# Kernel optimization log

Hardware: AMD Instinct MI355X
Metric: run time of the kernel (lower is better)

Reference implementation:

```python
import jax, jax.numpy as jnp
import numpy as np

D_IN = 512
D_OUT = 512
NUM_HEADS = 8
HEAD_DIM = D_OUT // NUM_HEADS


def setup_inputs() -> dict:
    key = jax.random.key(0)
    ks = jax.random.split(key, 6)
    b, t, n = 4, 32, 256
    scale = 1.0 / np.sqrt(D_IN)
    return {
        "x": jax.random.normal(ks[0], (b, t, n, D_IN), dtype=jnp.float32),
        "Wq": jax.random.normal(ks[1], (D_IN, D_OUT), dtype=jnp.float32) * scale,
        "Wk": jax.random.normal(ks[2], (D_IN, D_OUT), dtype=jnp.float32) * scale,
        "Wv": jax.random.normal(ks[3], (D_IN, D_OUT), dtype=jnp.float32) * scale,
        "Wo": jax.random.normal(ks[4], (D_OUT, D_OUT), dtype=jnp.float32) * scale,
        "bo": jax.random.normal(ks[5], (D_OUT,), dtype=jnp.float32) * 0.01,
    }


def reference(x, Wq, Wk, Wv, Wo, bo):
    b, t, n, _ = x.shape
    h, hd = NUM_HEADS, HEAD_DIM
    # QKV projections (no bias, qkv_bias=False)
    q = (x @ Wq).reshape(b, t, n, h, hd)
    k = (x @ Wk).reshape(b, t, n, h, hd)
    v = (x @ Wv).reshape(b, t, n, h, hd)
    # attention over tokens, per (batch, timestamp, head)
    scores = jnp.einsum('btqhd,btkhd->bthqk', q, k) / np.sqrt(hd).astype(jnp.float32)
    weights = jax.nn.softmax(scores, axis=-1)
    # dropout p=0.0 (eval / deterministic reference) -> identity
    ctx = jnp.einsum('bthqk,btkhd->btqhd', weights, v).reshape(b, t, n, D_OUT)
    return ctx @ Wo + bo
```

## Files before the change

kernel.cpp:

```cpp
#include <hip/hip_runtime.h>
#include <hip/hip_bf16.h>

typedef __attribute__((ext_vector_type(8))) short bf16x8;
typedef __attribute__((ext_vector_type(4))) float f32x4;

#define MFMA_16x16x32(a,b,c) __builtin_amdgcn_mfma_f32_16x16x32_bf16((a),(b),(c),0,0,0)

__device__ __forceinline__ unsigned short f2bf(float f){
  unsigned int u = __float_as_uint(f);
  u += 0x7FFFu + ((u >> 16) & 1u);
  return (unsigned short)(u >> 16);
}

__device__ __forceinline__ unsigned int cvtpk_bf16(float lo, float hi){
  unsigned int r;
  asm("v_cvt_pk_bf16_f32 %0, %1, %2" : "=v"(r) : "v"(lo), "v"(hi));
  return r;
}

__device__ __forceinline__ void async16(const void* g, void* l){
  __builtin_amdgcn_global_load_lds((const __attribute__((address_space(1))) void*)g,
                                   (__attribute__((address_space(3))) void*)l,
                                   16, 0, 0);
}

#define FENCE asm volatile("" ::: "memory")
#define BARR  do{ FENCE; __builtin_amdgcn_s_barrier(); FENCE; }while(0)

__global__ __launch_bounds__(256) void convert_x_kernel(const float* __restrict__ x,
                                                        unsigned short* __restrict__ xb, int n4){
  int idx = blockIdx.x*256 + threadIdx.x;
  int stride = gridDim.x*256;
  for (int i = idx; i < n4; i += stride){
    float4 v = reinterpret_cast<const float4*>(x)[i];
    ushort4 o;
    o.x = f2bf(v.x); o.y = f2bf(v.y); o.z = f2bf(v.z); o.w = f2bf(v.w);
    reinterpret_cast<ushort4*>(xb)[i] = o;
  }
}

__global__ __launch_bounds__(256) void prep_weights(const float* __restrict__ Wq,
                                                    const float* __restrict__ Wk,
                                                    const float* __restrict__ Wv,
                                                    const float* __restrict__ Wo,
                                                    unsigned short* __restrict__ WqkvT,
                                                    unsigned short* __restrict__ WoT){
  int idx = blockIdx.x*256 + threadIdx.x;
  int stride = gridDim.x*256;
  const int T1 = 1536*512;
  const int total = T1 + 512*512;
  for (int o = idx; o < total; o += stride){
    if (o < T1){
      int n = o >> 9, k = o & 511;
      const float* W = (n < 512) ? Wq : ((n < 1024) ? Wk : Wv);
      WqkvT[o] = f2bf(W[k*512 + (n & 511)]);
    } else {
      int o2 = o - T1;
      int n = o2 >> 9, k = o2 & 511;
      WoT[o2] = f2bf(Wo[k*512 + n]);
    }
  }
}

template<bool BIAS, bool OUTBF16>
__global__ __launch_bounds__(512, 2) void gemm8(const unsigned short* __restrict__ A,
                                                const unsigned short* __restrict__ Bt,
                                                float* __restrict__ Cf, unsigned short* __restrict__ Cb,
                                                const float* __restrict__ bias,
                                                int K, int NB, int ldc){
  __shared__ __attribute__((aligned(16))) char ldsA[2][32768];
  __shared__ __attribute__((aligned(16))) char ldsB[2][32768];
  const int tid = threadIdx.x;
  const int lane = tid & 63, w = tid >> 6;
  const int wr = w >> 2, wc = w & 3;
  const int l15 = lane & 15, lhi = lane >> 4;
  const int xorv = (l15 & 7) << 4;

  const int cpx = gridDim.x >> 3;
  const int bid = (blockIdx.x & 7) * cpx + (blockIdx.x >> 3);
  const int bm = bid / NB, bn = bid % NB;

  const int row0 = tid >> 3;
  const int srcb = ((tid & 7) << 4) ^ ((row0 & 7) << 4);
  const size_t rK2 = (size_t)K * 2;
  const char* Ab = (const char*)(A + (size_t)(bm*256 + row0) * K) + srcb;
  const char* Bb = (const char*)(Bt + (size_t)(bn*256 + row0) * K) + srcb;

#define STG_A(p,h,kt) do{ \
    async16(Ab + (size_t)((h)*128)*rK2      + (size_t)(kt)*2, ldsA[p] + (h)*16384 +        w*1024); \
    async16(Ab + (size_t)((h)*128 + 64)*rK2 + (size_t)(kt)*2, ldsA[p] + (h)*16384 + 8192 + w*1024); }while(0)
#define STG_B(p,h,kt) do{ \
    async16(Bb + (size_t)((h)*128)*rK2      + (size_t)(kt)*2, ldsB[p] + (h)*16384 +        w*1024); \
    async16(Bb + (size_t)((h)*128 + 64)*rK2 + (size_t)(kt)*2, ldsB[p] + (h)*16384 + 8192 + w*1024); }while(0)

#define LDAF(p, mh) do{ _Pragma("unroll") for (int f=0;f<4;++f){ \
    const char* base_ = ldsA[p] + (wr*128 + ((mh)*4+f)*16 + l15)*128; \
    af[f][0] = *reinterpret_cast<const bf16x8*>(base_ + (((lhi<<4))      ^ xorv)); \
    af[f][1] = *reinterpret_cast<const bf16x8*>(base_ + ((64 + (lhi<<4)) ^ xorv)); } }while(0)
#define LDBF(dst, p, nh) do{ _Pragma("unroll") for (int n2=0;n2<2;++n2){ \
    const char* base_ = ldsB[p] + (wc*64 + ((nh)*2+n2)*16 + l15)*128; \
    dst[n2][0] = *reinterpret_cast<const bf16x8*>(base_ + (((lhi<<4))      ^ xorv)); \
    dst[n2][1] = *reinterpret_cast<const bf16x8*>(base_ + ((64 + (lhi<<4)) ^ xorv)); } }while(0)
#define MFQ(mh, nh, B_) do{ _Pragma("unroll") for (int f=0;f<4;++f) \
    _Pragma("unroll") for (int n2=0;n2<2;++n2) \
    _Pragma("unroll") for (int kk=0;kk<2;++kk) \
      acc[(mh)*4+f][(nh)*2+n2] = MFMA_16x16x32(af[f][kk], B_[n2][kk], acc[(mh)*4+f][(nh)*2+n2]); }while(0)

  f32x4 acc[8][4];
  const f32x4 fzero = {0.f,0.f,0.f,0.f};
  #pragma unroll
  for (int i=0;i<8;++i)
    #pragma unroll
    for (int j=0;j<4;++j) acc[i][j] = fzero;
  bf16x8 af[4][2], bf0[2][2], bfc[2][2];
  const int nt = K >> 6;

  STG_B(0,0,0);  STG_B(0,1,0);  STG_A(0,0,0);  STG_A(0,1,0);
  STG_B(1,0,64); STG_B(1,1,64);
  asm volatile("s_waitcnt vmcnt(4)" ::: "memory");
  __builtin_amdgcn_s_barrier(); FENCE;

  for (int t = 0; t < nt; ++t){
    const int p = t & 1, o = p ^ 1;
    const int kt1 = (t+1) << 6, kt2 = (t+2) << 6;
    LDAF(p, 0); LDBF(bf0, p, 0);
    if (t+1 < nt) STG_A(o, 0, kt1);
    BARR;
    __builtin_amdgcn_s_setprio(1); MFQ(0, 0, bf0); __builtin_amdgcn_s_setprio(0);
    BARR;
    LDBF(bfc, p, 1);
    if (t+1 < nt) STG_A(o, 1, kt1);
    BARR;
    __builtin_amdgcn_s_setprio(1); MFQ(0, 1, bfc); __builtin_amdgcn_s_setprio(0);
    BARR;
    LDAF(p, 1);
    if (t+2 < nt) STG_B(p, 0, kt2);
    BARR;
    __builtin_amdgcn_s_setprio(1); MFQ(1, 1, bfc); __builtin_amdgcn_s_setprio(0);
    BARR;
    if (t+2 < nt) STG_B(p, 1, kt2);
    BARR;
    __builtin_amdgcn_s_setprio(1); MFQ(1, 0, bf0); __builtin_amdgcn_s_setprio(0);
    if (t+1 < nt){
      if (t+2 < nt) asm volatile("s_waitcnt vmcnt(4)" ::: "memory");
      else          asm volatile("s_waitcnt vmcnt(0)" ::: "memory");
      __builtin_amdgcn_s_barrier(); FENCE;
    }
  }

  #pragma unroll
  for (int mi=0;mi<8;++mi){
    const int r = bm*256 + wr*128 + mi*16 + lhi*4;
    #pragma unroll
    for (int ni=0;ni<4;++ni){
      const int cc = bn*256 + wc*64 + ni*16 + l15;
      float bv = 0.f;
      if (BIAS) bv = bias[cc];
      #pragma unroll
      for (int i=0;i<4;++i){
        float v = acc[mi][ni][i] + bv;
        if (OUTBF16) Cb[(size_t)(r+i)*ldc + cc] = f2bf(v);
        else         Cf[(size_t)(r+i)*ldc + cc] = v;
      }
    }
  }
#undef STG_A
#undef STG_B
#undef LDAF
#undef LDBF
#undef MFQ
}

__global__ __launch_bounds__(256) void attn_kernel(const unsigned short* __restrict__ qkv,
                                                   unsigned short* __restrict__ ctx){
  __shared__ __attribute__((aligned(16))) unsigned short Ks[256*64];
  __shared__ __attribute__((aligned(16))) unsigned short Vst[64*264];

  const int bid = blockIdx.x;
  const int h = bid & 7, bt = bid >> 3;
  const int r0 = bt << 8;
  const int tid = threadIdx.x;
  const int lane = tid & 63, w = tid >> 6;
  const int l15 = lane & 15, lhi = lane >> 4;
  const char* qkvB = (const char*)qkv;
  const f32x4 fzero = {0.f,0.f,0.f,0.f};

  bf16x8 qf[4][2];
  #pragma unroll
  for (int st=0; st<4; ++st){
    int q0 = w*64 + st*16;
    #pragma unroll
    for (int kk=0; kk<2; ++kk)
      qf[st][kk] = *reinterpret_cast<const bf16x8*>(
          qkvB + ((size_t)(r0 + q0 + l15)*1536 + h*64 + kk*32 + lhi*8)*2);
  }

  #pragma unroll
  for (int j=0;j<8;++j){
    int c = (w*8+j)*64 + lane;
    int tok = c >> 3;
    int src = ((c & 7) << 4) ^ ((tok & 7) << 4);
    async16(qkvB + ((size_t)(r0 + tok)*1536 + 512 + h*64)*2 + src,
            (char*)Ks + ((w*8+j) << 10));
  }
  {
    const char* vbase = qkvB + ((size_t)(r0 + tid)*1536 + 1024 + h*64)*2;
    #pragma unroll
    for (int j=0;j<8;++j){
      bf16x8 vv = *reinterpret_cast<const bf16x8*>(vbase + (j<<4));
      #pragma unroll
      for (int e=0;e<8;++e)
        Vst[(j*8+e)*264 + tid] = (unsigned short)vv[e];
    }
  }
  __syncthreads();

  const int ga2 = (lhi & 1) << 1;
  const int lA = l15 + (ga2 << 4);
  const int lB = lA + 16;
  const bool odd = (lhi >> 1) != 0;

  #pragma unroll
  for (int st=0; st<4; ++st){
    const int q0 = w*64 + st*16;

    f32x4 S[16];
    #pragma unroll
    for (int t=0;t<16;++t) S[t] = fzero;
    #pragma unroll
    for (int kk=0;kk<2;++kk){
      #pragma unroll
      for (int t=0;t<16;++t){
        int tok = t*16 + l15;
        int off = tok*128 + (((kk<<6) + (lhi<<4)) ^ ((tok & 7) << 4));
        bf16x8 kf = *reinterpret_cast<const bf16x8*>((const char*)Ks + off);
        S[t] = MFMA_16x16x32(kf, qf[st][kk], S[t]);
      }
    }

    float m = S[0][0];
    #pragma unroll
    for (int t=0;t<16;++t)
      #pragma unroll
      for (int i=0;i<4;++i) m = fmaxf(m, S[t][i]);
    m = fmaxf(m, __shfl_xor(m, 16));
    m = fmaxf(m, __shfl_xor(m, 32));

    float l = 0.f;
    unsigned int P2[32];
    #pragma unroll
    for (int t=0;t<16;++t){
      float p0 = __expf((S[t][0] - m) * 0.125f);
      float p1 = __expf((S[t][1] - m) * 0.125f);
      float p2 = __expf((S[t][2] - m) * 0.125f);
      float p3 = __expf((S[t][3] - m) * 0.125f);
      l += (p0 + p1) + (p2 + p3);
      P2[2*t]   = cvtpk_bf16(p0, p1);
      P2[2*t+1] = cvtpk_bf16(p2, p3);
    }
    l += __shfl_xor(l, 16);
    l += __shfl_xor(l, 32);
    float rl = 1.0f / l;

    f32x4 O[4];
    #pragma unroll
    for (int dt=0;dt<4;++dt) O[dt] = fzero;
    #pragma unroll
    for (int s=0;s<8;++s){
      unsigned int a0e = __shfl((int)P2[4*s+0], lA), a0o = __shfl((int)P2[4*s+2], lA);
      unsigned int a1e = __shfl((int)P2[4*s+1], lA), a1o = __shfl((int)P2[4*s+3], lA);
      unsigned int b0e = __shfl((int)P2[4*s+0], lB), b0o = __shfl((int)P2[4*s+2], lB);
      unsigned int b1e = __shfl((int)P2[4*s+1], lB), b1o = __shfl((int)P2[4*s+3], lB);
      unsigned int u0 = odd ? a0o : a0e;
      unsigned int u1 = odd ? a1o : a1e;
      unsigned int u2 = odd ? b0o : b0e;
      unsigned int u3 = odd ? b1o : b1e;
      bf16x8 pa;
      reinterpret_cast<unsigned int*>(&pa)[0] = u0;
      reinterpret_cast<unsigned int*>(&pa)[1] = u1;
      reinterpret_cast<unsigned int*>(&pa)[2] = u2;
      reinterpret_cast<unsigned int*>(&pa)[3] = u3;
      #pragma unroll
      for (int dt=0;dt<4;++dt){
        bf16x8 vb = *reinterpret_cast<const bf16x8*>(&Vst[(dt*16 + l15)*264 + s*32 + 8*lhi]);
        O[dt] = MFMA_16x16x32(pa, vb, O[dt]);
      }
    }

    float rl4[4];
    #pragma unroll
    for (int i=0;i<4;++i) rl4[i] = __shfl(rl, lhi*4 + i);
    #pragma unroll
    for (int dt=0;dt<4;++dt){
      int col = h*64 + dt*16 + l15;
      #pragma unroll
      for (int i=0;i<4;++i){
        int row = r0 + q0 + lhi*4 + i;
        ctx[(size_t)row*512 + col] = f2bf(O[dt][i] * rl4[i]);
      }
    }
  }
}

extern "C" void kernel_launch(void* const* d_in, const int* in_sizes, int n_in,
                              void* d_out, int out_size, void* d_ws, size_t ws_size,
                              hipStream_t stream) {
  const float* x  = (const float*)d_in[0];
  const float* Wq = (const float*)d_in[1];
  const float* Wk = (const float*)d_in[2];
  const float* Wv = (const float*)d_in[3];
  const float* Wo = (const float*)d_in[4];
  const float* bo = (const float*)d_in[5];
  float* out = (float*)d_out;

  char* ws = (char*)d_ws;
  unsigned short* xb    = (unsigned short*)ws;
  unsigned short* qkv   = (unsigned short*)(ws + 33554432);
  unsigned short* WqkvT = (unsigned short*)(ws + 134217728);
  unsigned short* WoT   = (unsigned short*)(ws + 135790592);
  unsigned short* ctx   = xb;

  convert_x_kernel<<<2048, 256, 0, stream>>>(x, xb, 16777216/4);
  prep_weights<<<1024, 256, 0, stream>>>(Wq, Wk, Wv, Wo, WqkvT, WoT);
  gemm8<false, true><<<768, 512, 0, stream>>>(xb, WqkvT, nullptr, qkv, nullptr, 512, 6, 1536);
  attn_kernel<<<1024, 256, 0, stream>>>(qkv, ctx);
  gemm8<true, false><<<256, 512, 0, stream>>>(ctx, WoT, out, nullptr, bo, 512, 2, 512);
}
```

Baseline: 168.4 us.

## Merge conversion kernels and use smaller-tile GEMM for output projection

Merges the x conversion and the weight transpose/convert into one kernel, saving a launch. Replaces the output-projection gemm8 (256 blocks of 512 threads) with a new 128x128-tile gemm_bt launched as 1024 blocks of 256 threads. The smaller tiles are meant to spread the output GEMM across more CUs. The new GEMM is single-buffered, with a sync between load and compute, so it gives up the pipelining the original kernel likely had.

```diff
diff --git a/kernel.cpp b/kernel.cpp
--- a/kernel.cpp
+++ b/kernel.cpp
@@ -27,26 +27,23 @@
 #define FENCE asm volatile("" ::: "memory")
 #define BARR  do{ FENCE; __builtin_amdgcn_s_barrier(); FENCE; }while(0)
 
-__global__ __launch_bounds__(256) void convert_x_kernel(const float* __restrict__ x,
-                                                        unsigned short* __restrict__ xb, int n4){
+__global__ __launch_bounds__(256) void convert_all(const float* __restrict__ x,
+                                                   const float* __restrict__ Wq,
+                                                   const float* __restrict__ Wk,
+                                                   const float* __restrict__ Wv,
+                                                   const float* __restrict__ Wo,
+                                                   unsigned short* __restrict__ xb,
+                                                   unsigned short* __restrict__ WqkvT,
+                                                   unsigned short* __restrict__ WoT){
   int idx = blockIdx.x*256 + threadIdx.x;
   int stride = gridDim.x*256;
+  const int n4 = 16777216/4;
   for (int i = idx; i < n4; i += stride){
     float4 v = reinterpret_cast<const float4*>(x)[i];
     ushort4 o;
     o.x = f2bf(v.x); o.y = f2bf(v.y); o.z = f2bf(v.z); o.w = f2bf(v.w);
     reinterpret_cast<ushort4*>(xb)[i] = o;
   }
-}
-
-__global__ __launch_bounds__(256) void prep_weights(const float* __restrict__ Wq,
-                                                    const float* __restrict__ Wk,
-                                                    const float* __restrict__ Wv,
-                                                    const float* __restrict__ Wo,
-                                                    unsigned short* __restrict__ WqkvT,
-                                                    unsigned short* __restrict__ WoT){
-  int idx = blockIdx.x*256 + threadIdx.x;
-  int stride = gridDim.x*256;
   const int T1 = 1536*512;
   const int total = T1 + 512*512;
   for (int o = idx; o < total; o += stride){
@@ -169,6 +166,89 @@
 #undef LDAF
 #undef LDBF
 #undef MFQ
+}
+
+template<bool BIAS, bool OUTBF16>
+__global__ __launch_bounds__(256) void gemm_bt(const unsigned short* __restrict__ A,
+                                               const unsigned short* __restrict__ Bt,
+                                               float* __restrict__ Cf, unsigned short* __restrict__ Cb,
+                                               const float* __restrict__ bias,
+                                               int M, int N, int K, int ldc){
+  __shared__ __attribute__((aligned(16))) unsigned short As[128*64];
+  __shared__ __attribute__((aligned(16))) unsigned short Bs[128*64];
+  const int tid = threadIdx.x;
+  const int lane = tid & 63;
+  const int w = tid >> 6;
+  const int l15 = lane & 15, lhi = lane >> 4;
+  const int NB = N >> 7;
+  const int bm = blockIdx.x / NB;
+  const int bn = blockIdx.x % NB;
+  const int wr = w >> 1, wc = w & 1;
+  const f32x4 fzero = {0.f,0.f,0.f,0.f};
+
+  f32x4 acc[4][4];
+  #pragma unroll
+  for (int a=0;a<4;++a)
+    #pragma unroll
+    for (int b=0;b<4;++b) acc[a][b] = fzero;
+
+  for (int kt = 0; kt < K; kt += 64){
+    #pragma unroll
+    for (int j=0;j<4;++j){
+      int c = (w*4+j)*64 + lane;
+      int row = c >> 3;
+      int src = ((c & 7) << 4) ^ ((row & 7) << 4);
+      async16((const char*)(A + (size_t)(bm*128 + row)*K + kt) + src,
+              (char*)As + ((w*4+j) << 10));
+    }
+    #pragma unroll
+    for (int j=0;j<4;++j){
+      int c = (w*4+j)*64 + lane;
+      int row = c >> 3;
+      int src = ((c & 7) << 4) ^ ((row & 7) << 4);
+      async16((const char*)(Bt + (size_t)(bn*128 + row)*K + kt) + src,
+              (char*)Bs + ((w*4+j) << 10));
+    }
+    __syncthreads();
+    #pragma unroll
+    for (int kk=0;kk<2;++kk){
+      bf16x8 af[4], bfr[4];
+      #pragma unroll
+      for (int mi=0;mi<4;++mi){
+        int m = wr*64 + mi*16 + l15;
+        int off = m*128 + (((kk<<6) + (lhi<<4)) ^ ((m & 7) << 4));
+        af[mi] = *reinterpret_cast<const bf16x8*>((const char*)As + off);
+      }
+      #pragma unroll
+      for (int ni=0;ni<4;++ni){
+        int n = wc*64 + ni*16 + l15;
+        int off = n*128 + (((kk<<6) + (lhi<<4)) ^ ((n & 7) << 4));
+        bfr[ni] = *reinterpret_cast<const bf16x8*>((const char*)Bs + off);
+      }
+      #pragma unroll
+      for (int mi=0;mi<4;++mi)
+        #pragma unroll
+        for (int ni=0;ni<4;++ni)
+          acc[mi][ni] = MFMA_16x16x32(af[mi], bfr[ni], acc[mi][ni]);
+    }
+    __syncthreads();
+  }
+  #pragma unroll
+  for (int mi=0;mi<4;++mi){
+    int r = bm*128 + wr*64 + mi*16 + lhi*4;
+    #pragma unroll
+    for (int ni=0;ni<4;++ni){
+      int cc = bn*128 + wc*64 + ni*16 + l15;
+      float bv = 0.f;
+      if (BIAS) bv = bias[cc];
+      #pragma unroll
+      for (int i=0;i<4;++i){
+        float v = acc[mi][ni][i] + bv;
+        if (OUTBF16) Cb[(size_t)(r+i)*ldc + cc] = f2bf(v);
+        else         Cf[(size_t)(r+i)*ldc + cc] = v;
+      }
+    }
+  }
 }
 
 __global__ __launch_bounds__(256) void attn_kernel(const unsigned short* __restrict__ qkv,
@@ -320,9 +400,9 @@
   unsigned short* WoT   = (unsigned short*)(ws + 135790592);
   unsigned short* ctx   = xb;
 
-  convert_x_kernel<<<2048, 256, 0, stream>>>(x, xb, 16777216/4);
-  prep_weights<<<1024, 256, 0, stream>>>(Wq, Wk, Wv, Wo, WqkvT, WoT);
+  convert_all<<<2048, 256, 0, stream>>>(x, Wq, Wk, Wv, Wo, xb, WqkvT, WoT);
   gemm8<false, true><<<768, 512, 0, stream>>>(xb, WqkvT, nullptr, qkv, nullptr, 512, 6, 1536);
   attn_kernel<<<1024, 256, 0, stream>>>(qkv, ctx);
-  gemm8<true, false><<<256, 512, 0, stream>>>(ctx, WoT, out, nullptr, bo, 512, 2, 512);
-}
+  gemm_bt<true, false><<<1024, 256, 0, stream>>>(ctx, WoT, out, nullptr, bo,
+                                                 32768, 512, 512, 512);
+}
```

New measurement: 172.6 us. 1.02x slower.

## Shrink GEMM tiles to 128x128 with 4 waves and fuse conversion kernels

Applied to the files above, without the earlier changes.

Replaces the 256x256-tile, 8-wave GEMM with a 128x128-tile, 4-wave version that has a simpler two-phase pipeline per K step and fewer barriers. Grids grow to 3072 and 1024 blocks to improve load balance and occupancy across CUs. It also merges the x conversion and weight preparation into one launch. The trade-off is less data reuse per tile and more global/L2 traffic.

```diff
diff --git a/kernel.cpp b/kernel.cpp
--- a/kernel.cpp
+++ b/kernel.cpp
@@ -26,27 +26,26 @@
 
 #define FENCE asm volatile("" ::: "memory")
 #define BARR  do{ FENCE; __builtin_amdgcn_s_barrier(); FENCE; }while(0)
-
-__global__ __launch_bounds__(256) void convert_x_kernel(const float* __restrict__ x,
-                                                        unsigned short* __restrict__ xb, int n4){
+#define BARRL do{ asm volatile("s_waitcnt lgkmcnt(0)" ::: "memory"); \
+                  __builtin_amdgcn_s_barrier(); FENCE; }while(0)
+
+__global__ __launch_bounds__(256) void convert_all(const float* __restrict__ x,
+                                                   const float* __restrict__ Wq,
+                                                   const float* __restrict__ Wk,
+                                                   const float* __restrict__ Wv,
+                                                   const float* __restrict__ Wo,
+                                                   unsigned short* __restrict__ xb,
+                                                   unsigned short* __restrict__ WqkvT,
+                                                   unsigned short* __restrict__ WoT){
   int idx = blockIdx.x*256 + threadIdx.x;
   int stride = gridDim.x*256;
+  const int n4 = 16777216/4;
   for (int i = idx; i < n4; i += stride){
     float4 v = reinterpret_cast<const float4*>(x)[i];
     ushort4 o;
     o.x = f2bf(v.x); o.y = f2bf(v.y); o.z = f2bf(v.z); o.w = f2bf(v.w);
     reinterpret_cast<ushort4*>(xb)[i] = o;
   }
-}
-
-__global__ __launch_bounds__(256) void prep_weights(const float* __restrict__ Wq,
-                                                    const float* __restrict__ Wk,
-                                                    const float* __restrict__ Wv,
-                                                    const float* __restrict__ Wo,
-                                                    unsigned short* __restrict__ WqkvT,
-                                                    unsigned short* __restrict__ WoT){
-  int idx = blockIdx.x*256 + threadIdx.x;
-  int stride = gridDim.x*256;
   const int T1 = 1536*512;
   const int total = T1 + 512*512;
   for (int o = idx; o < total; o += stride){
@@ -63,16 +62,16 @@
 }
 
 template<bool BIAS, bool OUTBF16>
-__global__ __launch_bounds__(512, 2) void gemm8(const unsigned short* __restrict__ A,
+__global__ __launch_bounds__(256, 2) void gemm4(const unsigned short* __restrict__ A,
                                                 const unsigned short* __restrict__ Bt,
                                                 float* __restrict__ Cf, unsigned short* __restrict__ Cb,
                                                 const float* __restrict__ bias,
                                                 int K, int NB, int ldc){
-  __shared__ __attribute__((aligned(16))) char ldsA[2][32768];
-  __shared__ __attribute__((aligned(16))) char ldsB[2][32768];
+  __shared__ __attribute__((aligned(16))) char ldsA[2][16384];
+  __shared__ __attribute__((aligned(16))) char ldsB[2][16384];
   const int tid = threadIdx.x;
   const int lane = tid & 63, w = tid >> 6;
-  const int wr = w >> 2, wc = w & 3;
+  const int wr = w >> 1, wc = w & 1;
   const int l15 = lane & 15, lhi = lane >> 4;
   const int xorv = (l15 & 7) << 4;
 
@@ -83,77 +82,65 @@
   const int row0 = tid >> 3;
   const int srcb = ((tid & 7) << 4) ^ ((row0 & 7) << 4);
   const size_t rK2 = (size_t)K * 2;
-  const char* Ab = (const char*)(A + (size_t)(bm*256 + row0) * K) + srcb;
-  const char* Bb = (const char*)(Bt + (size_t)(bn*256 + row0) * K) + srcb;
-
-#define STG_A(p,h,kt) do{ \
-    async16(Ab + (size_t)((h)*128)*rK2      + (size_t)(kt)*2, ldsA[p] + (h)*16384 +        w*1024); \
-    async16(Ab + (size_t)((h)*128 + 64)*rK2 + (size_t)(kt)*2, ldsA[p] + (h)*16384 + 8192 + w*1024); }while(0)
-#define STG_B(p,h,kt) do{ \
-    async16(Bb + (size_t)((h)*128)*rK2      + (size_t)(kt)*2, ldsB[p] + (h)*16384 +        w*1024); \
-    async16(Bb + (size_t)((h)*128 + 64)*rK2 + (size_t)(kt)*2, ldsB[p] + (h)*16384 + 8192 + w*1024); }while(0)
-
-#define LDAF(p, mh) do{ _Pragma("unroll") for (int f=0;f<4;++f){ \
-    const char* base_ = ldsA[p] + (wr*128 + ((mh)*4+f)*16 + l15)*128; \
-    af[f][0] = *reinterpret_cast<const bf16x8*>(base_ + (((lhi<<4))      ^ xorv)); \
-    af[f][1] = *reinterpret_cast<const bf16x8*>(base_ + ((64 + (lhi<<4)) ^ xorv)); } }while(0)
+  const char* Ab = (const char*)(A + (size_t)(bm*128 + row0) * K) + srcb;
+  const char* Bb = (const char*)(Bt + (size_t)(bn*128 + row0) * K) + srcb;
+
+#define STG_A(p,kt) do{ _Pragma("unroll") for (int j=0;j<4;++j) \
+    async16(Ab + (size_t)(j*32)*rK2 + (size_t)(kt)*2, ldsA[p] + j*4096 + w*1024); }while(0)
+#define STG_B(p,kt) do{ _Pragma("unroll") for (int j=0;j<4;++j) \
+    async16(Bb + (size_t)(j*32)*rK2 + (size_t)(kt)*2, ldsB[p] + j*4096 + w*1024); }while(0)
+
+#define LDAF(p) do{ _Pragma("unroll") for (int f=0;f<4;++f){ \
+    const char* base_ = ldsA[p] + (wr*64 + f*16 + l15)*128; \
+    const int m_ = wr*64 + f*16 + l15; \
+    af[f][0] = *reinterpret_cast<const bf16x8*>(base_ + (((lhi<<4))      ^ ((m_&7)<<4))); \
+    af[f][1] = *reinterpret_cast<const bf16x8*>(base_ + ((64 + (lhi<<4)) ^ ((m_&7)<<4))); } }while(0)
 #define LDBF(dst, p, nh) do{ _Pragma("unroll") for (int n2=0;n2<2;++n2){ \
-    const char* base_ = ldsB[p] + (wc*64 + ((nh)*2+n2)*16 + l15)*128; \
-    dst[n2][0] = *reinterpret_cast<const bf16x8*>(base_ + (((lhi<<4))      ^ xorv)); \
-    dst[n2][1] = *reinterpret_cast<const bf16x8*>(base_ + ((64 + (lhi<<4)) ^ xorv)); } }while(0)
-#define MFQ(mh, nh, B_) do{ _Pragma("unroll") for (int f=0;f<4;++f) \
+    const int n_ = wc*64 + ((nh)*2+n2)*16 + l15; \
+    const char* base_ = ldsB[p] + n_*128; \
+    dst[n2][0] = *reinterpret_cast<const bf16x8*>(base_ + (((lhi<<4))      ^ ((n_&7)<<4))); \
+    dst[n2][1] = *reinterpret_cast<const bf16x8*>(base_ + ((64 + (lhi<<4)) ^ ((n_&7)<<4))); } }while(0)
+#define MFQ(nh, B_) do{ _Pragma("unroll") for (int f=0;f<4;++f) \
     _Pragma("unroll") for (int n2=0;n2<2;++n2) \
     _Pragma("unroll") for (int kk=0;kk<2;++kk) \
-      acc[(mh)*4+f][(nh)*2+n2] = MFMA_16x16x32(af[f][kk], B_[n2][kk], acc[(mh)*4+f][(nh)*2+n2]); }while(0)
-
-  f32x4 acc[8][4];
+      acc[f][(nh)*2+n2] = MFMA_16x16x32(af[f][kk], B_[n2][kk], acc[f][(nh)*2+n2]); }while(0)
+
+  f32x4 acc[4][4];
   const f32x4 fzero = {0.f,0.f,0.f,0.f};
   #pragma unroll
-  for (int i=0;i<8;++i)
+  for (int i=0;i<4;++i)
     #pragma unroll
     for (int j=0;j<4;++j) acc[i][j] = fzero;
   bf16x8 af[4][2], bf0[2][2], bfc[2][2];
   const int nt = K >> 6;
 
-  STG_B(0,0,0);  STG_B(0,1,0);  STG_A(0,0,0);  STG_A(0,1,0);
-  STG_B(1,0,64); STG_B(1,1,64);
+  STG_A(0,0); STG_B(0,0); STG_B(1,64);
   asm volatile("s_waitcnt vmcnt(4)" ::: "memory");
   __builtin_amdgcn_s_barrier(); FENCE;
 
   for (int t = 0; t < nt; ++t){
     const int p = t & 1, o = p ^ 1;
     const int kt1 = (t+1) << 6, kt2 = (t+2) << 6;
-    LDAF(p, 0); LDBF(bf0, p, 0);
-    if (t+1 < nt) STG_A(o, 0, kt1);
+    LDAF(p); LDBF(bf0, p, 0); LDBF(bfc, p, 1);
+    if (t+1 < nt) STG_A(o, kt1);
     BARR;
-    __builtin_amdgcn_s_setprio(1); MFQ(0, 0, bf0); __builtin_amdgcn_s_setprio(0);
-    BARR;
-    LDBF(bfc, p, 1);
-    if (t+1 < nt) STG_A(o, 1, kt1);
-    BARR;
-    __builtin_amdgcn_s_setprio(1); MFQ(0, 1, bfc); __builtin_amdgcn_s_setprio(0);
-    BARR;
-    LDAF(p, 1);
-    if (t+2 < nt) STG_B(p, 0, kt2);
-    BARR;
-    __builtin_amdgcn_s_setprio(1); MFQ(1, 1, bfc); __builtin_amdgcn_s_setprio(0);
-    BARR;
-    if (t+2 < nt) STG_B(p, 1, kt2);
-    BARR;
-    __builtin_amdgcn_s_setprio(1); MFQ(1, 0, bf0); __builtin_amdgcn_s_setprio(0);
+    __builtin_amdgcn_s_setprio(1); MFQ(0, bf0); __builtin_amdgcn_s_setprio(0);
+    BARRL;
+    if (t+2 < nt) STG_B(p, kt2);
+    __builtin_amdgcn_s_setprio(1); MFQ(1, bfc); __builtin_amdgcn_s_setprio(0);
     if (t+1 < nt){
-      if (t+2 < nt) asm volatile("s_waitcnt vmcnt(4)" ::: "memory");
-      else          asm volatile("s_waitcnt vmcnt(0)" ::: "memory");
+      if (t+2 < nt) asm volatile("s_waitcnt vmcnt(4) lgkmcnt(0)" ::: "memory");
+      else          asm volatile("s_waitcnt vmcnt(0) lgkmcnt(0)" ::: "memory");
       __builtin_amdgcn_s_barrier(); FENCE;
     }
   }
 
   #pragma unroll
-  for (int mi=0;mi<8;++mi){
-    const int r = bm*256 + wr*128 + mi*16 + lhi*4;
+  for (int mi=0;mi<4;++mi){
+    const int r = bm*128 + wr*64 + mi*16 + lhi*4;
     #pragma unroll
     for (int ni=0;ni<4;++ni){
-      const int cc = bn*256 + wc*64 + ni*16 + l15;
+      const int cc = bn*128 + wc*64 + ni*16 + l15;
       float bv = 0.f;
       if (BIAS) bv = bias[cc];
       #pragma unroll
@@ -320,9 +307,8 @@
   unsigned short* WoT   = (unsigned short*)(ws + 135790592);
   unsigned short* ctx   = xb;
 
-  convert_x_kernel<<<2048, 256, 0, stream>>>(x, xb, 16777216/4);
-  prep_weights<<<1024, 256, 0, stream>>>(Wq, Wk, Wv, Wo, WqkvT, WoT);
-  gemm8<false, true><<<768, 512, 0, stream>>>(xb, WqkvT, nullptr, qkv, nullptr, 512, 6, 1536);
+  convert_all<<<2048, 256, 0, stream>>>(x, Wq, Wk, Wv, Wo, xb, WqkvT, WoT);
+  gemm4<false, true><<<3072, 256, 0, stream>>>(xb, WqkvT, nullptr, qkv, nullptr, 512, 12, 1536);
   attn_kernel<<<1024, 256, 0, stream>>>(qkv, ctx);
-  gemm8<true, false><<<256, 512, 0, stream>>>(ctx, WoT, out, nullptr, bo, 512, 2, 512);
-}
+  gemm4<true, false><<<1024, 256, 0, stream>>>(ctx, WoT, out, nullptr, bo, 512, 4, 512);
+}
```

Result: faster. 165.0 us (-2.0%).
